# Optimization experiments

Hardware: AMD Instinct MI355X
Metric: run time of the kernel (lower is better)

The kernel has to match this reference:

```python
import jax, jax.numpy as jnp
import numpy as np

PNS = (1, 2, 3, 4, 6, 8, 12, 16)
N_E, E_DIM = 8192, 256
BETA = 0.25
ALPHA = 0.5  # abs(quant_resi)
B, HW = 64, 16


def _area_mat(out_n, in_n):
    # torch adaptive_avg_pool1d matrix (F.interpolate mode='area')
    M = np.zeros((out_n, in_n), np.float32)
    for i in range(out_n):
        s = (i * in_n) // out_n
        e = -((-(i + 1) * in_n) // out_n)  # ceil((i+1)*in_n/out_n)
        M[i, s:e] = 1.0 / (e - s)
    return M


def _cubic_w(t):
    a = -0.75  # torch bicubic coefficient
    t = abs(t)
    if t <= 1.0:
        return (a + 2) * t ** 3 - (a + 3) * t ** 2 + 1.0
    if t < 2.0:
        return a * t ** 3 - 5 * a * t ** 2 + 8 * a * t - 4 * a
    return 0.0


def _bicubic_mat(out_n, in_n):
    # torch F.interpolate mode='bicubic', align_corners=False, border-replicate taps
    M = np.zeros((out_n, in_n), np.float32)
    scale = in_n / out_n
    for i in range(out_n):
        x = (i + 0.5) * scale - 0.5
        f = int(np.floor(x))
        for k in range(-1, 3):
            idx = min(max(f + k, 0), in_n - 1)
            M[i, idx] += _cubic_w(x - (f + k))
    return M


def setup_inputs() -> dict:
    key = jax.random.key(0)
    k1, k2, k3 = jax.random.split(key, 3)
    z = jax.random.normal(k1, (B, E_DIM, HW, HW), jnp.float32)
    embedding = jax.random.normal(k2, (N_E, E_DIM), jnp.float32)
    conv_w = jax.random.normal(k3, (len(PNS), E_DIM, E_DIM, 3, 3), jnp.float32) * 0.02
    conv_b = jnp.zeros((len(PNS), E_DIM), jnp.float32)
    return {"z": z, "embedding": embedding, "conv_w": conv_w, "conv_b": conv_b}


def reference(z, embedding, conv_w, conv_b):
    Bz, C, H, W = z.shape
    S = len(PNS)
    z_rest = z
    z_hat = jnp.zeros_like(z)
    total_loss = jnp.zeros((), z.dtype)
    counts = jnp.zeros((N_E,), z.dtype)
    e_sq = jnp.sum(embedding ** 2, axis=1)  # [n_e]
    for si, pn in enumerate(PNS):
        if si != S - 1:
            A = jnp.asarray(_area_mat(pn, H))
            zd = jnp.einsum('ph,qw,bchw->bpqc', A, A, z_rest)  # [B,pn,pn,C]
        else:
            zd = jnp.transpose(z_rest, (0, 2, 3, 1))
        zf = zd.reshape(-1, C)  # [N,C]
        dist = jnp.sum(zf ** 2, axis=1, keepdims=True) + e_sq - 2.0 * (zf @ embedding.T)
        idx = jnp.argmin(dist, axis=1)  # [N]
        zk = embedding[idx].reshape(zd.shape)  # [B,pn,pn,C]
        zk = jnp.transpose(zk, (0, 3, 1, 2))  # [B,C,pn,pn]
        if si != S - 1:
            U = jnp.asarray(_bicubic_mat(H, pn))
            zu = jnp.einsum('hp,wq,bcpq->bchw', U, U, zk)
        else:
            zu = zk
        y = jax.lax.conv_general_dilated(
            zu, conv_w[si], (1, 1), 'SAME',
            dimension_numbers=('NCHW', 'OIHW', 'NCHW')) + conv_b[si][None, :, None, None]
        res = zu * (1.0 - ALPHA) + y * ALPHA
        z_hat = z_hat + res
        z_rest = z_rest - res
        counts = counts.at[idx].add(jnp.asarray(1.0, z.dtype))
        total_loss = total_loss + BETA * jnp.mean((jax.lax.stop_gradient(z_hat) - z) ** 2)
    mean_vq_loss = total_loss / S
    z_hat_out = z + jax.lax.stop_gradient(z_hat - z)
    return z_hat_out, mean_vq_loss, counts
```

## Files before the change

kernel.cpp:

```cpp
#include <hip/hip_runtime.h>
#include <math.h>

#define NB 64
#define NC 256
#define NHW 16
#define NE 8192
#define NUMEL 4194304
#define LOSS_OFF 4194304
#define CNT_OFF  4194305

typedef __bf16 bf16x8 __attribute__((ext_vector_type(8)));
typedef float  f32x4  __attribute__((ext_vector_type(4)));

#define GLOAD_LDS(gptr, lptr) \
  __builtin_amdgcn_global_load_lds( \
      (const __attribute__((address_space(1))) unsigned int*)(gptr), \
      (__attribute__((address_space(3))) unsigned int*)(lptr), 16, 0, 0)

__device__ __forceinline__ float cubicw(float t) {
  t = fabsf(t);
  if (t <= 1.0f) return (1.25f * t - 2.25f) * t * t + 1.0f;
  if (t < 2.0f)  return ((-0.75f * t + 3.75f) * t - 6.0f) * t + 3.0f;
  return 0.0f;
}

__device__ __forceinline__ short f2bf(float x) {
  union { float f; unsigned int u; } v; v.f = x;
  unsigned int r = v.u + 0x7fffu + ((v.u >> 16) & 1u);
  return (short)(r >> 16);
}
__device__ __forceinline__ float bf2f(short h) {
  union { float f; unsigned int u; } v;
  v.u = ((unsigned int)(unsigned short)h) << 16;
  return v.f;
}

__global__ void k_zero(float* a, int na) {
  int i = blockIdx.x * 256 + threadIdx.x;
  if (i < na) a[i] = 0.0f;
}

__global__ void k_tr_in(const float* __restrict__ z, float* __restrict__ zrest) {
  int n = blockIdx.x, c = threadIdx.x;
  int b = n >> 8, hw = n & 255;
  zrest[(size_t)n * 256 + c] = z[((size_t)(b * 256 + c)) * 256 + hw];
}

__global__ void k_prep_emb2(const float* __restrict__ emb, short* __restrict__ B2,
                            float* __restrict__ esq) {
  int j = blockIdx.x, t = threadIdx.x;
  float v = emb[(size_t)j * 256 + t];
  short hi = f2bf(v);
  short lo = f2bf(v - bf2f(hi));
  B2[(size_t)j * 768 + t]       = hi;
  B2[(size_t)j * 768 + 256 + t] = hi;
  B2[(size_t)j * 768 + 512 + t] = lo;
  __shared__ float red[256];
  red[t] = v * v;
  __syncthreads();
  for (int s = 128; s > 0; s >>= 1) { if (t < s) red[t] += red[t + s]; __syncthreads(); }
  if (t == 0) esq[j] = red[0];
}

__global__ void k_prep_wb(const float* __restrict__ w, short* __restrict__ wB2) {
  int m = blockIdx.x * 256 + threadIdx.x;
  if (m >= 8 * 9 * 65536) return;
  int i = m & 255, o = (m >> 8) & 255;
  int r = m >> 16;
  int si = r / 9, tap = r % 9;
  float v = w[(((size_t)si * 256 + o) * 256 + i) * 9 + tap];
  short hi = f2bf(v);
  short lo = f2bf(v - bf2f(hi));
  size_t dst = ((size_t)r * 256 + o) * 768;
  wB2[dst + i]       = hi;
  wB2[dst + 256 + i] = hi;
  wB2[dst + 512 + i] = lo;
}

__global__ void k_down_a2(const float* __restrict__ zrest, short* __restrict__ A2, int pn) {
  int pq = blockIdx.x, b = blockIdx.y, c = threadIdx.x;
  int p = pq / pn, q = pq % pn;
  int sp = (p * 16) / pn, ep = ((p + 1) * 16 + pn - 1) / pn;
  int sq = (q * 16) / pn, eq = ((q + 1) * 16 + pn - 1) / pn;
  float s = 0.0f;
  for (int h = sp; h < ep; h++)
    for (int w = sq; w < eq; w++)
      s += zrest[((size_t)((b * 16 + h) * 16 + w)) * 256 + c];
  float x = s / (float)((ep - sp) * (eq - sq));
  int n = (b * pn + p) * pn + q;
  short hi = f2bf(x);
  short lo = f2bf(x - bf2f(hi));
  A2[(size_t)n * 768 + c]       = hi;
  A2[(size_t)n * 768 + 256 + c] = lo;
  A2[(size_t)n * 768 + 512 + c] = hi;
}

__global__ void k_split_a2(const float* __restrict__ zrest, short* __restrict__ A2) {
  int n = blockIdx.x, c = threadIdx.x;
  float x = zrest[(size_t)n * 256 + c];
  short hi = f2bf(x);
  short lo = f2bf(x - bf2f(hi));
  A2[(size_t)n * 768 + c]       = hi;
  A2[(size_t)n * 768 + 256 + c] = lo;
  A2[(size_t)n * 768 + 512 + c] = hi;
}

__global__ __launch_bounds__(512, 2) void k_dist_mfma(
    const short* __restrict__ A2, const short* __restrict__ B2,
    const float* __restrict__ esq, float* __restrict__ pd, int* __restrict__ pi,
    int N) {
  __shared__ short As[4][8192];
  __shared__ short Bs[4][8192];
  int t = threadIdx.x, ln = t & 63, wv = t >> 6;
  int wr = wv >> 2, wc = wv & 3;
  int n0 = blockIdx.x * 256;
  int jb0 = blockIdx.y * 256;
  int lc = ln & 15, lq = ln >> 4;

  const short* gA[2]; const short* gB[2]; int ldst[2];
#pragma unroll
  for (int i = 0; i < 2; i++) {
    int C = i * 512 + wv * 64 + ln;
    int L = C >> 3, c5s = C & 7;
    int c5g = c5s ^ (L & 7);
    int rowg = (L << 1) | (c5g >> 2), ccg = c5g & 3;
    gA[i] = A2 + (size_t)(n0 + rowg) * 768 + ccg * 8;
    gB[i] = B2 + (size_t)(jb0 + rowg) * 768 + ccg * 8;
    ldst[i] = (i * 512 + wv * 64) * 8;
  }
  int offA[2][4], offB[4];
#pragma unroll
  for (int rt = 0; rt < 4; rt++) {
#pragma unroll
    for (int h = 0; h < 2; h++) {
      int row = wr * 128 + h * 64 + rt * 16 + lc;
      int L = row >> 1;
      int swc = (((row & 1) << 2) + lq) ^ (L & 7);
      offA[h][rt] = L * 64 + swc * 8;
    }
    int rowb = wc * 64 + rt * 16 + lc;
    int Lb = rowb >> 1;
    int swb = (((rowb & 1) << 2) + lq) ^ (Lb & 7);
    offB[rt] = Lb * 64 + swb * 8;
  }

  f32x4 acc[8][4];
#pragma unroll
  for (int at = 0; at < 8; at++)
#pragma unroll
    for (int ac = 0; ac < 4; ac++) acc[at][ac] = (f32x4)(0.0f);

#define DSTAGE(tile_, bsel_)                                          \
  {                                                                   \
    _Pragma("unroll")                                                 \
    for (int i = 0; i < 2; i++)                                       \
      GLOAD_LDS(gA[i] + (tile_) * 32, &As[(bsel_)][ldst[i]]);         \
    _Pragma("unroll")                                                 \
    for (int i = 0; i < 2; i++)                                       \
      GLOAD_LDS(gB[i] + (tile_) * 32, &Bs[(bsel_)][ldst[i]]);         \
  }

  DSTAGE(0, 0);
  DSTAGE(1, 1);
  DSTAGE(2, 2);
  asm volatile("s_waitcnt vmcnt(8)" ::: "memory");
  __builtin_amdgcn_s_barrier();

#pragma unroll
  for (int kt = 0; kt < 24; kt++) {
    const int bsel = kt & 3;
    const short* aBase = &As[bsel][0];
    const short* bBase = &Bs[bsel][0];
    if (kt < 21) DSTAGE(kt + 3, (kt + 3) & 3);
    bf16x8 fa0[4], fb[4];
#pragma unroll
    for (int rt = 0; rt < 4; rt++)
      fa0[rt] = *(const bf16x8*)(aBase + offA[0][rt]);
#pragma unroll
    for (int ct = 0; ct < 4; ct++)
      fb[ct] = *(const bf16x8*)(bBase + offB[ct]);
    __builtin_amdgcn_s_barrier();
    __builtin_amdgcn_s_setprio(1);
#pragma unroll
    for (int rt = 0; rt < 4; rt++)
#pragma unroll
      for (int ct = 0; ct < 4; ct++)
        acc[rt][ct] = __builtin_amdgcn_mfma_f32_16x16x32_bf16(
            fa0[rt], fb[ct], acc[rt][ct], 0, 0, 0);
    __builtin_amdgcn_s_setprio(0);
    __builtin_amdgcn_s_barrier();
    bf16x8 fa1[4];
#pragma unroll
    for (int rt = 0; rt < 4; rt++)
      fa1[rt] = *(const bf16x8*)(aBase + offA[1][rt]);
    __builtin_amdgcn_s_barrier();
    __builtin_amdgcn_s_setprio(1);
#pragma unroll
    for (int rt = 0; rt < 4; rt++)
#pragma unroll
      for (int ct = 0; ct < 4; ct++)
        acc[4 + rt][ct] = __builtin_amdgcn_mfma_f32_16x16x32_bf16(
            fa1[rt], fb[ct], acc[4 + rt][ct], 0, 0, 0);
    __builtin_amdgcn_s_setprio(0);
    if (kt < 23) {
      if (kt < 21)       { asm volatile("s_waitcnt vmcnt(8)" ::: "memory"); }
      else if (kt == 21) { asm volatile("s_waitcnt vmcnt(4)" ::: "memory"); }
      else               { asm volatile("s_waitcnt vmcnt(0)" ::: "memory"); }
      __builtin_amdgcn_s_barrier();
    }
  }
#undef DSTAGE

  float* sbd = (float*)(&As[0][0]);
  int*   sbi = (int*)((char*)(&As[0][0]) + 4096);

#pragma unroll
  for (int at = 0; at < 8; at++) {
    float bst[4]; int bix[4];
#pragma unroll
    for (int r = 0; r < 4; r++) { bst[r] = 3.4e38f; bix[r] = 0; }
#pragma unroll
    for (int ac = 0; ac < 4; ac++) {
      int j = jb0 + wc * 64 + ac * 16 + lc;
      float es = esq[j];
#pragma unroll
      for (int r = 0; r < 4; r++) {
        float d = es - 2.0f * acc[at][ac][r];
        if (d < bst[r]) { bst[r] = d; bix[r] = j; }
      }
    }
#pragma unroll
    for (int r = 0; r < 4; r++) {
      float bd = bst[r]; int bi = bix[r];
#pragma unroll
      for (int off = 1; off < 16; off <<= 1) {
        float od = __shfl_xor(bd, off, 64);
        int   oi = __shfl_xor(bi, off, 64);
        if (od < bd || (od == bd && oi < bi)) { bd = od; bi = oi; }
      }
      if (lc == 0) {
        int rl = wr * 128 + at * 16 + lq * 4 + r;
        sbd[wc * 256 + rl] = bd;
        sbi[wc * 256 + rl] = bi;
      }
    }
  }
  __syncthreads();
  if (t < 256) {
    float b0 = sbd[t]; int i0 = sbi[t];
#pragma unroll
    for (int w = 1; w < 4; w++) {
      float b1 = sbd[w * 256 + t]; int i1 = sbi[w * 256 + t];
      if (b1 < b0 || (b1 == b0 && i1 < i0)) { b0 = b1; i0 = i1; }
    }
    int n = n0 + t;
    if (n < N) {
      pd[(size_t)n * 32 + blockIdx.y] = b0;
      pi[(size_t)n * 32 + blockIdx.y] = i0;
    }
  }
}

__global__ void k_red(const float* __restrict__ pd, const int* __restrict__ pi,
                      int* __restrict__ idxb, float* __restrict__ counts, int N, int nct) {
  int n = blockIdx.x * 256 + threadIdx.x;
  if (n >= N) return;
  float bd = pd[(size_t)n * nct]; int bi = pi[(size_t)n * nct];
  for (int jt = 1; jt < nct; jt++) {
    float d = pd[(size_t)n * nct + jt]; int ii = pi[(size_t)n * nct + jt];
    if (d < bd || (d == bd && ii < bi)) { bd = d; bi = ii; }
  }
  idxb[n] = bi;
  atomicAdd(counts + bi, 1.0f);
}

__global__ void k_up(const float* __restrict__ emb, const int* __restrict__ idxb,
                     float* __restrict__ zu, short* __restrict__ zu2, int pn, int last) {
  int n = blockIdx.x, c = threadIdx.x;
  float acc;
  if (last) {
    acc = emb[(size_t)idxb[n] * 256 + c];
  } else {
    int b = n >> 8, hw = n & 255, h = hw >> 4, w = hw & 15;
    float scale = pn / 16.0f;
    float xh = (h + 0.5f) * scale - 0.5f; int fh = (int)floorf(xh);
    float xw = (w + 0.5f) * scale - 0.5f; int fw = (int)floorf(xw);
    int ph[4], pw[4]; float wh[4], wwt[4];
#pragma unroll
    for (int k = 0; k < 4; k++) {
      wh[k] = cubicw(xh - (float)(fh + k - 1));
      int pp = fh + k - 1; ph[k] = min(max(pp, 0), pn - 1);
      wwt[k] = cubicw(xw - (float)(fw + k - 1));
      pp = fw + k - 1; pw[k] = min(max(pp, 0), pn - 1);
    }
    acc = 0.0f;
#pragma unroll
    for (int kh = 0; kh < 4; kh++)
#pragma unroll
      for (int kw = 0; kw < 4; kw++) {
        int row = idxb[(n >> 8) * pn * pn + ph[kh] * pn + pw[kw]];
        acc += wh[kh] * wwt[kw] * emb[(size_t)row * 256 + c];
      }
  }
  zu[(size_t)n * 256 + c] = acc;
  short hi = f2bf(acc);
  short lo = f2bf(acc - bf2f(hi));
  zu2[(size_t)n * 768 + c]       = hi;
  zu2[(size_t)n * 768 + 256 + c] = lo;
  zu2[(size_t)n * 768 + 512 + c] = hi;
}

__global__ __launch_bounds__(512, 2) void k_conv_mfma(
    const short* __restrict__ zu2, const short* __restrict__ wB2,
    const float* __restrict__ cb, const float* __restrict__ zu,
    float* __restrict__ zrest, float* __restrict__ out_loss, int si) {
  __shared__ short Ah[2][108 * 64];
  __shared__ short Bs[3][256 * 64];
  __shared__ float red[512];
  int t = threadIdx.x, ln = t & 63, wv = t >> 6;
  int pxh = wv >> 2, oq = wv & 3;
  int lc = ln & 15, lq = ln >> 4;
  int b = blockIdx.x >> 2, h0 = (blockIdx.x & 3) * 4;

  bool awr[2], aval[2]; const short* asrc[2]; int adst[2];
#pragma unroll
  for (int i = 0; i < 2; i++) {
    int c = t * 2 + i;
    int rh = c >> 3, cc = c & 7;
    int hh = rh / 18, wx = rh - hh * 18;
    int h = h0 + hh - 1, w = wx - 1;
    awr[i]  = (c < 864);
    aval[i] = awr[i] && (h >= 0) && (h < 16) && (w >= 0) && (w < 16);
    int n = aval[i] ? (b * 256 + h * 16 + w) : 0;
    asrc[i] = zu2 + (size_t)n * 768 + cc * 8;
    adst[i] = rh * 64 + (cc ^ (rh & 7)) * 8;
  }

#define CSTAGE(nt_, nk_, bsel_)                                             \
  {                                                                         \
    const short* bbase =                                                    \
        wB2 + (((size_t)si * 9 + (nt_)) * 256) * 768 + (nk_) * 64;          \
    _Pragma("unroll")                                                       \
    for (int i = 0; i < 4; i++) {                                           \
      int Lb = i * 512 + wv * 64;                                           \
      int L = Lb + ln;                                                      \
      int row = L >> 3, cc = L & 7;                                         \
      int gc = cc ^ (row & 7);                                              \
      GLOAD_LDS(bbase + (size_t)row * 768 + gc * 8, &Bs[(bsel_)][Lb * 8]);  \
    }                                                                       \
  }

  f32x4 acc[2][4];
#pragma unroll
  for (int pf = 0; pf < 2; pf++)
#pragma unroll
    for (int ct = 0; ct < 4; ct++) acc[pf][ct] = (f32x4)(0.0f);

  {
    CSTAGE(0, 0, 0);
    CSTAGE(1, 0, 1);
    uint4 a0 = make_uint4(0u, 0u, 0u, 0u), a1 = make_uint4(0u, 0u, 0u, 0u);
    if (aval[0]) a0 = *(const uint4*)(asrc[0]);
    if (aval[1]) a1 = *(const uint4*)(asrc[1]);
    if (awr[0]) *(uint4*)(&Ah[0][adst[0]]) = a0;
    if (awr[1]) *(uint4*)(&Ah[0][adst[1]]) = a1;
    asm volatile("s_waitcnt vmcnt(4) lgkmcnt(0)" ::: "memory");
  }
  __builtin_amdgcn_s_barrier();

  for (int kc = 0; kc < 12; kc++) {
    int ab = kc & 1;
    uint4 na0 = make_uint4(0u, 0u, 0u, 0u), na1 = make_uint4(0u, 0u, 0u, 0u);
#pragma unroll
    for (int tap = 0; tap < 9; tap++) {
      const int rb3 = tap % 3;
      const int sb3 = (tap + 2) % 3;
      int dh = tap / 3 - 1, dw = tap % 3 - 1;
      bf16x8 fa[2][2], fb[2][4];
#pragma unroll
      for (int ks = 0; ks < 2; ks++) {
#pragma unroll
        for (int pf = 0; pf < 2; pf++) {
          int rh = (pxh * 2 + pf + dh + 1) * 18 + lc + dw + 1;
          int cc = (ks * 4 + lq) ^ (rh & 7);
          fa[ks][pf] = *(const bf16x8*)(&Ah[ab][rh * 64 + cc * 8]);
        }
#pragma unroll
        for (int ct = 0; ct < 4; ct++) {
          int row = oq * 64 + ct * 16 + lc;
          int cc = (ks * 4 + lq) ^ (lc & 7);
          fb[ks][ct] = *(const bf16x8*)(&Bs[rb3][row * 64 + cc * 8]);
        }
      }
      if (kc < 11 || tap < 7) {
        int nt = (tap < 7) ? tap + 2 : tap - 7;
        int nk = (tap < 7) ? kc : kc + 1;
        CSTAGE(nt, nk, sb3);
      }
      if (tap == 0 && kc < 11) {
        int koff = (kc + 1) * 64;
        if (aval[0]) na0 = *(const uint4*)(asrc[0] + koff);
        if (aval[1]) na1 = *(const uint4*)(asrc[1] + koff);
      }
      if (tap == 8 && kc < 11) {
        if (awr[0]) *(uint4*)(&Ah[ab ^ 1][adst[0]]) = na0;
        if (awr[1]) *(uint4*)(&Ah[ab ^ 1][adst[1]]) = na1;
      }
      __builtin_amdgcn_s_barrier();
      __builtin_amdgcn_s_setprio(1);
#pragma unroll
      for (int ks = 0; ks < 2; ks++)
#pragma unroll
        for (int pf = 0; pf < 2; pf++)
#pragma unroll
          for (int ct = 0; ct < 4; ct++)
            acc[pf][ct] = __builtin_amdgcn_mfma_f32_16x16x32_bf16(
                fa[ks][pf], fb[ks][ct], acc[pf][ct], 0, 0, 0);
      __builtin_amdgcn_s_setprio(0);
      if (tap == 8) {
        if (kc < 11) {
          asm volatile("s_waitcnt vmcnt(4) lgkmcnt(0)" ::: "memory");
          __builtin_amdgcn_s_barrier();
        }
      } else if (tap == 7) {
        if (kc < 11) { asm volatile("s_waitcnt vmcnt(4)" ::: "memory"); }
        else         { asm volatile("s_waitcnt vmcnt(0)" ::: "memory"); }
        __builtin_amdgcn_s_barrier();
      } else {
        asm volatile("s_waitcnt vmcnt(4)" ::: "memory");
        __builtin_amdgcn_s_barrier();
      }
    }
  }
#undef CSTAGE
  __syncthreads();

  float lsum = 0.0f;
#pragma unroll
  for (int ct = 0; ct < 4; ct++) {
    int o = oq * 64 + ct * 16 + lc;
    float bias = cb[si * 256 + o];
#pragma unroll
    for (int pf = 0; pf < 2; pf++) {
      int n = b * 256 + (h0 + pxh * 2 + pf) * 16;
#pragma unroll
      for (int r = 0; r < 4; r++) {
        size_t m = (size_t)(n + lq * 4 + r) * 256 + o;
        float y = acc[pf][ct][r] + bias;
        float res = 0.5f * (zu[m] + y);
        float nv = zrest[m] - res;
        zrest[m] = nv;
        lsum += nv * nv;
      }
    }
  }
  red[t] = lsum;
  __syncthreads();
  for (int s = 256; s > 0; s >>= 1) { if (t < s) red[t] += red[t + s]; __syncthreads(); }
  if (t == 0) atomicAdd(out_loss, red[0] * (0.25f / (8.0f * 4194304.0f)));
}

__global__ void k_out(const float* __restrict__ z, const float* __restrict__ zrest,
                      float* __restrict__ out) {
  int n = blockIdx.x, c = threadIdx.x;
  int b = n >> 8, hw = n & 255;
  size_t m = ((size_t)(b * 256 + c)) * 256 + hw;
  out[m] = z[m] - zrest[(size_t)n * 256 + c];
}

extern "C" void kernel_launch(void* const* d_in, const int* in_sizes, int n_in,
                              void* d_out, int out_size, void* d_ws, size_t ws_size,
                              hipStream_t stream) {
  const float* z   = (const float*)d_in[0];
  const float* emb = (const float*)d_in[1];
  const float* cw  = (const float*)d_in[2];
  const float* cb  = (const float*)d_in[3];
  float* out = (float*)d_out;
  float* ws  = (float*)d_ws;

  float* z_rest = ws;
  float* zu     = ws + 4194304;
  float* esq    = ws + 8388608;
  short* A2     = (short*)(ws + 8396800);
  short* zu2    = A2;
  short* B2     = (short*)(ws + 14688256);
  short* wB2    = (short*)(ws + 17833984);
  float* pd     = ws + 24911872;
  int*   pi     = (int*)(ws + 25436160);
  int*   idxb   = (int*)(ws + 25960448);

  const int pns[8] = {1, 2, 3, 4, 6, 8, 12, 16};

  k_zero<<<33, 256, 0, stream>>>(out + LOSS_OFF, 1 + NE);
  k_tr_in<<<16384, 256, 0, stream>>>(z, z_rest);
  k_prep_emb2<<<8192, 256, 0, stream>>>(emb, B2, esq);
  k_prep_wb<<<18432, 256, 0, stream>>>(cw, wB2);

  for (int si = 0; si < 8; si++) {
    int pn = pns[si];
    int N = 64 * pn * pn;
    if (si < 7)
      k_down_a2<<<dim3(pn * pn, 64), 256, 0, stream>>>(z_rest, A2, pn);
    else
      k_split_a2<<<16384, 256, 0, stream>>>(z_rest, A2);
    int rb = (N + 255) / 256;
    k_dist_mfma<<<dim3(rb, 32), 512, 0, stream>>>(A2, B2, esq, pd, pi, N);
    k_red<<<(N + 255) / 256, 256, 0, stream>>>(pd, pi, idxb, out + CNT_OFF, N, 32);
    k_up<<<16384, 256, 0, stream>>>(emb, idxb, zu, zu2, pn, si == 7 ? 1 : 0);
    k_conv_mfma<<<dim3(256), 512, 0, stream>>>(zu2, wB2, cb, zu, z_rest,
                                               out + LOSS_OFF, si);
  }
  k_out<<<16384, 256, 0, stream>>>(z, z_rest, out);
}
```

Before: 1.997 ms.

## Cut dist kernel LDS to double-buffer and split conv over output-channel halves

The distance GEMM drops from a 4-deep to a 2-deep LDS ring and asks for 4 blocks per CU, so more blocks can be resident at the cost of a shallower prefetch that now waits for all loads each iteration. The conv kernel is split across a second grid dimension over output-channel halves, using 256-thread blocks with smaller weight staging buffers. That gives 512 blocks instead of 256 to fill the CUs, but each block reloads the same input tile and the vmcnt bookkeeping is retuned for four A loads per thread.

```diff
diff --git a/kernel.cpp b/kernel.cpp
--- a/kernel.cpp
+++ b/kernel.cpp
@@ -105,12 +105,12 @@
   A2[(size_t)n * 768 + 512 + c] = hi;
 }
 
-__global__ __launch_bounds__(512, 2) void k_dist_mfma(
+__global__ __launch_bounds__(512, 4) void k_dist_mfma(
     const short* __restrict__ A2, const short* __restrict__ B2,
     const float* __restrict__ esq, float* __restrict__ pd, int* __restrict__ pi,
     int N) {
-  __shared__ short As[4][8192];
-  __shared__ short Bs[4][8192];
+  __shared__ short As[2][8192];
+  __shared__ short Bs[2][8192];
   int t = threadIdx.x, ln = t & 63, wv = t >> 6;
   int wr = wv >> 2, wc = wv & 3;
   int n0 = blockIdx.x * 256;
@@ -161,17 +161,15 @@
   }
 
   DSTAGE(0, 0);
-  DSTAGE(1, 1);
-  DSTAGE(2, 2);
-  asm volatile("s_waitcnt vmcnt(8)" ::: "memory");
+  asm volatile("s_waitcnt vmcnt(0)" ::: "memory");
   __builtin_amdgcn_s_barrier();
 
 #pragma unroll
   for (int kt = 0; kt < 24; kt++) {
-    const int bsel = kt & 3;
+    const int bsel = kt & 1;
     const short* aBase = &As[bsel][0];
     const short* bBase = &Bs[bsel][0];
-    if (kt < 21) DSTAGE(kt + 3, (kt + 3) & 3);
+    if (kt < 23) DSTAGE(kt + 1, bsel ^ 1);
     bf16x8 fa0[4], fb[4];
 #pragma unroll
     for (int rt = 0; rt < 4; rt++)
@@ -203,9 +201,7 @@
             fa1[rt], fb[ct], acc[4 + rt][ct], 0, 0, 0);
     __builtin_amdgcn_s_setprio(0);
     if (kt < 23) {
-      if (kt < 21)       { asm volatile("s_waitcnt vmcnt(8)" ::: "memory"); }
-      else if (kt == 21) { asm volatile("s_waitcnt vmcnt(4)" ::: "memory"); }
-      else               { asm volatile("s_waitcnt vmcnt(0)" ::: "memory"); }
+      asm volatile("s_waitcnt vmcnt(0)" ::: "memory");
       __builtin_amdgcn_s_barrier();
     }
   }
@@ -310,22 +306,23 @@
   zu2[(size_t)n * 768 + 512 + c] = hi;
 }
 
-__global__ __launch_bounds__(512, 2) void k_conv_mfma(
+__global__ __launch_bounds__(256, 2) void k_conv_mfma(
     const short* __restrict__ zu2, const short* __restrict__ wB2,
     const float* __restrict__ cb, const float* __restrict__ zu,
     float* __restrict__ zrest, float* __restrict__ out_loss, int si) {
   __shared__ short Ah[2][108 * 64];
-  __shared__ short Bs[3][256 * 64];
-  __shared__ float red[512];
+  __shared__ short Bs[3][128 * 64];
+  __shared__ float red[256];
   int t = threadIdx.x, ln = t & 63, wv = t >> 6;
-  int pxh = wv >> 2, oq = wv & 3;
+  int pxh = wv >> 1, oq = wv & 1;
   int lc = ln & 15, lq = ln >> 4;
   int b = blockIdx.x >> 2, h0 = (blockIdx.x & 3) * 4;
-
-  bool awr[2], aval[2]; const short* asrc[2]; int adst[2];
-#pragma unroll
-  for (int i = 0; i < 2; i++) {
-    int c = t * 2 + i;
+  int o0 = blockIdx.y * 128;
+
+  bool awr[4], aval[4]; const short* asrc[4]; int adst[4];
+#pragma unroll
+  for (int i = 0; i < 4; i++) {
+    int c = i * 256 + t;
     int rh = c >> 3, cc = c & 7;
     int hh = rh / 18, wx = rh - hh * 18;
     int h = h0 + hh - 1, w = wx - 1;
@@ -339,10 +336,10 @@
 #define CSTAGE(nt_, nk_, bsel_)                                             \
   {                                                                         \
     const short* bbase =                                                    \
-        wB2 + (((size_t)si * 9 + (nt_)) * 256) * 768 + (nk_) * 64;          \
+        wB2 + (((size_t)si * 9 + (nt_)) * 256 + o0) * 768 + (nk_) * 64;     \
     _Pragma("unroll")                                                       \
     for (int i = 0; i < 4; i++) {                                           \
-      int Lb = i * 512 + wv * 64;                                           \
+      int Lb = i * 256 + wv * 64;                                           \
       int L = Lb + ln;                                                      \
       int row = L >> 3, cc = L & 7;                                         \
       int gc = cc ^ (row & 7);                                              \
@@ -357,20 +354,27 @@
     for (int ct = 0; ct < 4; ct++) acc[pf][ct] = (f32x4)(0.0f);
 
   {
+    uint4 a[4];
+#pragma unroll
+    for (int i = 0; i < 4; i++) {
+      a[i] = make_uint4(0u, 0u, 0u, 0u);
+      if (aval[i]) a[i] = *(const uint4*)(asrc[i]);
+    }
     CSTAGE(0, 0, 0);
     CSTAGE(1, 0, 1);
-    uint4 a0 = make_uint4(0u, 0u, 0u, 0u), a1 = make_uint4(0u, 0u, 0u, 0u);
-    if (aval[0]) a0 = *(const uint4*)(asrc[0]);
-    if (aval[1]) a1 = *(const uint4*)(asrc[1]);
-    if (awr[0]) *(uint4*)(&Ah[0][adst[0]]) = a0;
-    if (awr[1]) *(uint4*)(&Ah[0][adst[1]]) = a1;
+    asm volatile("s_waitcnt vmcnt(8)" ::: "memory");
+#pragma unroll
+    for (int i = 0; i < 4; i++)
+      if (awr[i]) *(uint4*)(&Ah[0][adst[i]]) = a[i];
     asm volatile("s_waitcnt vmcnt(4) lgkmcnt(0)" ::: "memory");
   }
   __builtin_amdgcn_s_barrier();
 
   for (int kc = 0; kc < 12; kc++) {
     int ab = kc & 1;
-    uint4 na0 = make_uint4(0u, 0u, 0u, 0u), na1 = make_uint4(0u, 0u, 0u, 0u);
+    uint4 na[4];
+#pragma unroll
+    for (int i = 0; i < 4; i++) na[i] = make_uint4(0u, 0u, 0u, 0u);
 #pragma unroll
     for (int tap = 0; tap < 9; tap++) {
       const int rb3 = tap % 3;
@@ -399,12 +403,14 @@
       }
       if (tap == 0 && kc < 11) {
         int koff = (kc + 1) * 64;
-        if (aval[0]) na0 = *(const uint4*)(asrc[0] + koff);
-        if (aval[1]) na1 = *(const uint4*)(asrc[1] + koff);
+#pragma unroll
+        for (int i = 0; i < 4; i++)
+          if (aval[i]) na[i] = *(const uint4*)(asrc[i] + koff);
       }
       if (tap == 8 && kc < 11) {
-        if (awr[0]) *(uint4*)(&Ah[ab ^ 1][adst[0]]) = na0;
-        if (awr[1]) *(uint4*)(&Ah[ab ^ 1][adst[1]]) = na1;
+#pragma unroll
+        for (int i = 0; i < 4; i++)
+          if (awr[i]) *(uint4*)(&Ah[ab ^ 1][adst[i]]) = na[i];
       }
       __builtin_amdgcn_s_barrier();
       __builtin_amdgcn_s_setprio(1);
@@ -417,18 +423,22 @@
             acc[pf][ct] = __builtin_amdgcn_mfma_f32_16x16x32_bf16(
                 fa[ks][pf], fb[ks][ct], acc[pf][ct], 0, 0, 0);
       __builtin_amdgcn_s_setprio(0);
-      if (tap == 8) {
-        if (kc < 11) {
-          asm volatile("s_waitcnt vmcnt(4) lgkmcnt(0)" ::: "memory");
-          __builtin_amdgcn_s_barrier();
-        }
+      if (tap <= 1) {
+        if (kc < 11) { asm volatile("s_waitcnt vmcnt(8)" ::: "memory"); }
+        else         { asm volatile("s_waitcnt vmcnt(4)" ::: "memory"); }
+        __builtin_amdgcn_s_barrier();
+      } else if (tap <= 6) {
+        asm volatile("s_waitcnt vmcnt(4)" ::: "memory");
+        __builtin_amdgcn_s_barrier();
       } else if (tap == 7) {
         if (kc < 11) { asm volatile("s_waitcnt vmcnt(4)" ::: "memory"); }
         else         { asm volatile("s_waitcnt vmcnt(0)" ::: "memory"); }
         __builtin_amdgcn_s_barrier();
       } else {
-        asm volatile("s_waitcnt vmcnt(4)" ::: "memory");
-        __builtin_amdgcn_s_barrier();
+        if (kc < 11) {
+          asm volatile("s_waitcnt vmcnt(4) lgkmcnt(0)" ::: "memory");
+          __builtin_amdgcn_s_barrier();
+        }
       }
     }
   }
@@ -438,7 +448,7 @@
   float lsum = 0.0f;
 #pragma unroll
   for (int ct = 0; ct < 4; ct++) {
-    int o = oq * 64 + ct * 16 + lc;
+    int o = o0 + oq * 64 + ct * 16 + lc;
     float bias = cb[si * 256 + o];
 #pragma unroll
     for (int pf = 0; pf < 2; pf++) {
@@ -456,7 +466,7 @@
   }
   red[t] = lsum;
   __syncthreads();
-  for (int s = 256; s > 0; s >>= 1) { if (t < s) red[t] += red[t + s]; __syncthreads(); }
+  for (int s = 128; s > 0; s >>= 1) { if (t < s) red[t] += red[t + s]; __syncthreads(); }
   if (t == 0) atomicAdd(out_loss, red[0] * (0.25f / (8.0f * 4194304.0f)));
 }
 
@@ -507,8 +517,8 @@
     k_dist_mfma<<<dim3(rb, 32), 512, 0, stream>>>(A2, B2, esq, pd, pi, N);
     k_red<<<(N + 255) / 256, 256, 0, stream>>>(pd, pi, idxb, out + CNT_OFF, N, 32);
     k_up<<<16384, 256, 0, stream>>>(emb, idxb, zu, zu2, pn, si == 7 ? 1 : 0);
-    k_conv_mfma<<<dim3(256), 512, 0, stream>>>(zu2, wB2, cb, zu, z_rest,
-                                               out + LOSS_OFF, si);
+    k_conv_mfma<<<dim3(256, 2), 256, 0, stream>>>(zu2, wB2, cb, zu, z_rest,
+                                                  out + LOSS_OFF, si);
   }
   k_out<<<16384, 256, 0, stream>>>(z, z_rest, out);
 }
```

Measured after the change: 5.458 ms. +173.3%, slower.
